# Performance work log

Measured on AMD Instinct MI355X. Metric: run time of the kernel, lower is better.

## Reference

```python
import jax, jax.numpy as jnp
import numpy as np

B, S, DA, DV, DU, L, M = 16, 256, 1, 32, 1, 4, 12


def conv1x1(x, w, b):
    # x: [B,C,H,W], w: [O,C], b: [O]
    return jnp.einsum('bchw,oc->bohw', x, w) + b[None, :, None, None]


def setup_inputs() -> dict:
    key = jax.random.key(0)
    ks = jax.random.split(key, 12)
    sc = 0.02
    return {
        'x':    jax.random.normal(ks[0], (B, S, S, DA), dtype=jnp.float32),
        'p_w':  sc * jax.random.normal(ks[1], (DV, DA + 2), dtype=jnp.float32),
        'p_b':  sc * jax.random.normal(ks[2], (DV,), dtype=jnp.float32),
        'ws_w': sc * jax.random.normal(ks[3], (L, DV, DV), dtype=jnp.float32),
        'ws_b': sc * jax.random.normal(ks[4], (L, DV), dtype=jnp.float32),
        'w1r':  sc * jax.random.normal(ks[5], (L, DV, DV, M, M), dtype=jnp.float32),
        'w1i':  sc * jax.random.normal(ks[6], (L, DV, DV, M, M), dtype=jnp.float32),
        'w2r':  sc * jax.random.normal(ks[7], (L, DV, DV, M, M), dtype=jnp.float32),
        'w2i':  sc * jax.random.normal(ks[8], (L, DV, DV, M, M), dtype=jnp.float32),
        'q_w':  sc * jax.random.normal(ks[9], (DU, DV), dtype=jnp.float32),
        'q_b':  sc * jax.random.normal(ks[10], (DU,), dtype=jnp.float32),
    }


def fourier_layer(x, w1r, w1i, w2r, w2i):
    # x: [B,C,H,W]; FFT norm None == 'backward' (numpy/jax default)
    b, c, h, w = x.shape
    x_ft = jnp.fft.rfft2(x)                       # [B,C,H,W//2+1] complex
    W1 = w1r + 1j * w1i                           # [C,C,M,M]
    W2 = w2r + 1j * w2i
    top = jnp.einsum('bixy,ioxy->boxy', x_ft[:, :, :M, :M], W1)
    bot = jnp.einsum('bixy,ioxy->boxy', x_ft[:, :, -M:, :M], W2)
    out_ft = jnp.zeros((b, c, h, w // 2 + 1), dtype=x_ft.dtype)
    out_ft = out_ft.at[:, :, :M, :M].set(top)
    out_ft = out_ft.at[:, :, h - M:, :M].set(bot)
    return jnp.fft.irfft2(out_ft, s=(h, w))


def reference(x, p_w, p_b, ws_w, ws_b, w1r, w1i, w2r, w2i, q_w, q_b):
    b, sx, sy, _ = x.shape
    # grid as in get_grid (requires sx == sy, as the original implicitly does)
    gx = jnp.linspace(-1.0, 1.0, sx, dtype=jnp.float32)
    gy = jnp.linspace(-1.0, 1.0, sy, dtype=jnp.float32)
    gridx = jnp.broadcast_to(gx.reshape(1, 1, sx, 1), (b, sy, sx, 1))
    gridy = jnp.broadcast_to(gy.reshape(1, sy, 1, 1), (b, sy, sx, 1))
    grid = jnp.concatenate([gridy, gridx], axis=-1)     # [B,Sy,Sx,2]
    h = jnp.concatenate([x, grid], axis=-1)             # [B,S,S,DA+2]
    h = jnp.transpose(h, (0, 3, 1, 2))                  # NCHW
    h = conv1x1(h, p_w, p_b)                            # lifting
    for i in range(L):
        x1 = fourier_layer(h, w1r[i], w1i[i], w2r[i], w2i[i])
        x2 = conv1x1(h, ws_w[i], ws_b[i])
        h = x1 + x2
        if i < L - 1:
            h = jax.nn.relu(h)
    h = conv1x1(h, q_w, q_b)                            # projection -> [B,1,S,S]
    return jnp.transpose(h, (0, 2, 3, 1)).squeeze(-1)   # [B,S,S]
```

## Files before the change

### kernel.cpp

```cpp
#include <hip/hip_runtime.h>
#include <math.h>

#define NB 16
#define SS 256
#define DV 32
#define MM 12
#define MK 24
#define LL 4
#define TWO_PI_N 0.024543692606170259679f


__global__ __launch_bounds__(256) void k_prep(const float* __restrict__ ws_w,
        float* __restrict__ twT, float* __restrict__ wT, float* __restrict__ tw2)
{
    int j = threadIdx.x;
    #pragma unroll
    for (int k = 0; k < MM; ++k) {
        float ang = TWO_PI_N * (float)((k * j) & 255);
        float s, c; sincosf(ang, &s, &c);
        twT[j * (MM * 2) + 2 * k]     = c;
        twT[j * (MM * 2) + 2 * k + 1] = -s;
        tw2[(k * SS + j) * 2]     = c;
        tw2[(k * SS + j) * 2 + 1] = s;
    }
    for (int idx = threadIdx.x; idx < LL * DV * DV; idx += 256) {
        int l = idx >> 10, rem = idx & 1023, co = rem >> 5, ci = rem & 31;
        wT[(l * DV + ci) * DV + co] = ws_w[(l * DV + co) * DV + ci];
    }
}

__global__ __launch_bounds__(256) void k_lift(const float* __restrict__ x,
        const float* __restrict__ p_w, const float* __restrict__ p_b,
        float* __restrict__ h)
{
    int tid = threadIdx.x;
    int lane = tid & 63;
    int w = __builtin_amdgcn_readfirstlane(tid >> 6);
    int b  = blockIdx.x >> 6;
    int iy = ((blockIdx.x & 63) << 2) + w;
    int j0 = lane << 2;

    float4 xv = *(const float4*)(x + ((size_t)(b * SS + iy)) * SS + j0);
    float gy = -1.f + 2.f * (float)iy * (1.f / 255.f);
    float4 gx;
    gx.x = -1.f + 2.f * (float)j0 * (1.f / 255.f);
    gx.y = gx.x + 2.f / 255.f; gx.z = gx.y + 2.f / 255.f; gx.w = gx.z + 2.f / 255.f;

    float* hb = h + ((size_t)b * DV * SS + iy) * SS + j0;
    #pragma unroll
    for (int c = 0; c < DV; ++c) {
        float w0 = p_w[3*c], w1 = p_w[3*c+1], w2 = p_w[3*c+2], bb = p_b[c];
        float4 v;
        v.x = w0 * xv.x + w1 * gy + w2 * gx.x + bb;
        v.y = w0 * xv.y + w1 * gy + w2 * gx.y + bb;
        v.z = w0 * xv.z + w1 * gy + w2 * gx.z + bb;
        v.w = w0 * xv.w + w1 * gy + w2 * gx.w + bb;
        *(float4*)(hb + (size_t)c * SS * SS) = v;
    }
}

__global__ __launch_bounds__(512, 4) void k_rowdft(const float* __restrict__ h,
        const float* __restrict__ twT, float* __restrict__ A)
{
    __shared__ float red[MM * 2][SS];
    int tid = threadIdx.x;
    int iy = tid & 255;
    int half = __builtin_amdgcn_readfirstlane(tid >> 8);
    int b = blockIdx.x >> 5, c = blockIdx.x & 31;

    const float4* hr = (const float4*)(h + ((size_t)blockIdx.x * SS + iy) * SS
                                         + half * 128);
    float ar[MM], ai[MM];
    #pragma unroll
    for (int k = 0; k < MM; ++k) { ar[k] = 0.f; ai[k] = 0.f; }

    #pragma unroll 4
    for (int j4 = 0; j4 < 32; ++j4) {
        float4 v = hr[j4];
        float vv[4] = {v.x, v.y, v.z, v.w};
        #pragma unroll
        for (int u = 0; u < 4; ++u) {
            const float* twj = twT + (size_t)(half * 128 + 4 * j4 + u) * (MM * 2);
            float vu = vv[u];
            #pragma unroll
            for (int k = 0; k < 6; ++k) {
                ar[2*k]   += vu * twj[4*k];
                ai[2*k]   += vu * twj[4*k + 1];
                ar[2*k+1] += vu * twj[4*k + 2];
                ai[2*k+1] += vu * twj[4*k + 3];
            }
        }
    }

    if (half == 0) {
        #pragma unroll
        for (int k = 0; k < MM; ++k) {
            red[2*k][iy]     = ar[k];
            red[2*k + 1][iy] = ai[k];
        }
    }
    __syncthreads();
    if (half == 1) {
        #pragma unroll
        for (int ky = 0; ky < MM; ++ky) {
            float2 val;
            val.x = ar[ky] + red[2*ky][iy];
            val.y = ai[ky] + red[2*ky + 1][iy];
            size_t o = ((((size_t)b * MM + ky) * DV + c) * SS + iy) * 2;
            *(float2*)&A[o] = val;
        }
    }
}

__global__ __launch_bounds__(256, 4) void k_cm(const float* __restrict__ A,
        const float* __restrict__ w1r, const float* __restrict__ w1i,
        const float* __restrict__ w2r, const float* __restrict__ w2i,
        float* __restrict__ F, int l)
{
    __shared__ float FinS[DV][6][2];
    int blk = blockIdx.x;
    int mg = blk & 3;
    int bk = blk >> 2;
    int ky = bk % MM;
    int tid = threadIdx.x;
    int c = tid >> 3, ch = tid & 7;
    int iy0 = ch * 32;

    const float2* Ap = (const float2*)(A + ((size_t)bk * DV + c) * SS * 2);

    float fr[6], fi[6], pc[6], ps[6], sc[6], ssn[6];
    #pragma unroll
    for (int k = 0; k < 6; ++k) {
        int m = mg * 6 + k;
        int f = (m < MM) ? m : (232 + m);
        float s, cc;
        sincosf(TWO_PI_N * (float)f, &s, &cc);
        sc[k] = cc; ssn[k] = s;
        sincosf(TWO_PI_N * (float)((f * iy0) & 255), &s, &cc);
        pc[k] = cc; ps[k] = s;
        fr[k] = fi[k] = 0.f;
    }
    #pragma unroll 4
    for (int i = 0; i < 32; ++i) {
        float2 a = Ap[iy0 + i];
        #pragma unroll
        for (int k = 0; k < 6; ++k) {
            fr[k] += a.x * pc[k] + a.y * ps[k];
            fi[k] += a.y * pc[k] - a.x * ps[k];
            float np = pc[k] * sc[k] - ps[k] * ssn[k];
            float nq = pc[k] * ssn[k] + ps[k] * sc[k];
            pc[k] = np; ps[k] = nq;
        }
    }
    #pragma unroll
    for (int m = 1; m < 8; m <<= 1) {
        #pragma unroll
        for (int k = 0; k < 6; ++k) {
            fr[k] += __shfl_xor(fr[k], m, 64);
            fi[k] += __shfl_xor(fi[k], m, 64);
        }
    }
    #pragma unroll
    for (int k = 0; k < 6; ++k) {
        if (ch == k) { FinS[c][k][0] = fr[k]; FinS[c][k][1] = fi[k]; }
    }
    __syncthreads();

    if (ch < 6) {
        int o = c;
        int m = mg * 6 + ch;
        const float* Wr; const float* Wi; int xm;
        if (m < MM) { Wr = w1r; Wi = w1i; xm = m; }
        else        { Wr = w2r; Wi = w2i; xm = m - MM; }
        float scale = ((ky == 0) ? 1.0f : 2.0f) * (1.0f / 65536.0f);
        float orr = 0.f, oii = 0.f;
        #pragma unroll 4
        for (int i = 0; i < DV; ++i) {
            float gr = FinS[i][ch][0], gi = FinS[i][ch][1];
            size_t wi = ((size_t)(l * DV + i) * DV + o) * (MM * MM) + xm * MM + ky;
            float wr = Wr[wi], wim = Wi[wi];
            orr += gr * wr - gi * wim;
            oii += gr * wim + gi * wr;
        }
        size_t off = (((size_t)bk * DV + o) * MK + m) * 2;
        F[off] = orr * scale; F[off + 1] = oii * scale;
    }
}

__global__ __launch_bounds__(384) void k_inv1(const float* __restrict__ F,
        float* __restrict__ g)
{
    __shared__ float itw[MK * 2];
    int tid = threadIdx.x;
    int b = blockIdx.x >> 8, iy = blockIdx.x & 255;
    if (tid < MK) {
        int f = (tid < MM) ? tid : (232 + tid);
        float ang = TWO_PI_N * (float)((f * iy) & 255);
        float s, c; sincosf(ang, &s, &c);
        itw[2 * tid] = c; itw[2 * tid + 1] = s;
    }
    __syncthreads();

    int ky = tid >> 5, co = tid & 31;
    const float2* Fp = (const float2*)(F + ((((size_t)b * MM + ky) * DV + co) * MK) * 2);
    float gr = 0.f, gi = 0.f;
    #pragma unroll
    for (int m = 0; m < MK; ++m) {
        float2 fv = Fp[m];
        float ic = itw[2 * m], is = itw[2 * m + 1];
        gr += fv.x * ic - fv.y * is;
        gi += fv.x * is + fv.y * ic;
    }
    size_t o = (((size_t)(b * SS + iy)) * MM + ky) * (DV * 2) + 2 * co;
    g[o] = gr; g[o + 1] = gi;
}

template<int FINAL>
__global__ __launch_bounds__(256, 4) void k_pt(float* __restrict__ h,
        const float* __restrict__ g, const float* __restrict__ wT,
        const float* __restrict__ ws_b, const float* __restrict__ tw2,
        const float* __restrict__ q_w, const float* __restrict__ q_b,
        float* __restrict__ out, int l)
{
    int tid = threadIdx.x;
    int lane = tid & 63;
    int w = __builtin_amdgcn_readfirstlane(tid >> 6);
    int b  = blockIdx.x >> 7;
    int iy = ((blockIdx.x & 127) << 1) + (w >> 1);
    int j0 = ((w & 1) << 7) + (lane << 1);

    float* hb = h + ((size_t)b * DV * SS + iy) * SS + j0;
    const float* wt  = wT + (size_t)l * DV * DV;
    const float* wsb = ws_b + (size_t)l * DV;

    float2 acc[DV];
    #pragma unroll
    for (int co = 0; co < DV; ++co) {
        float bv = wsb[co];
        acc[co].x = bv; acc[co].y = bv;
    }

    #pragma unroll 4
    for (int ci = 0; ci < DV; ++ci) {
        float2 hv = *(const float2*)(hb + (size_t)ci * SS * SS);
        const float* wc = wt + ci * DV;
        #pragma unroll
        for (int co = 0; co < DV; ++co) {
            float wv = wc[co];
            acc[co].x += wv * hv.x; acc[co].y += wv * hv.y;
        }
    }

    const float* gp = g + ((size_t)(b * SS + iy)) * (MM * DV * 2);
    #pragma unroll 2
    for (int ky = 0; ky < MM; ++ky) {
        float4 t4 = *(const float4*)(tw2 + ((size_t)ky * SS + j0) * 2);
        const float* Gk = gp + ky * (DV * 2);
        #pragma unroll
        for (int co = 0; co < DV; ++co) {
            float gr = Gk[2 * co], gi = Gk[2 * co + 1];
            acc[co].x += gr * t4.x - gi * t4.y;
            acc[co].y += gr * t4.z - gi * t4.w;
        }
    }

    if (FINAL) {
        float qb = q_b[0];
        float2 o2; o2.x = qb; o2.y = qb;
        #pragma unroll
        for (int co = 0; co < DV; ++co) {
            float qv = q_w[co];
            o2.x += qv * acc[co].x; o2.y += qv * acc[co].y;
        }
        *(float2*)(out + ((size_t)(b * SS + iy)) * SS + j0) = o2;
    } else {
        #pragma unroll
        for (int co = 0; co < DV; ++co) {
            float2 v;
            v.x = fmaxf(acc[co].x, 0.f); v.y = fmaxf(acc[co].y, 0.f);
            *(float2*)(hb + (size_t)co * SS * SS) = v;
        }
    }
}

extern "C" void kernel_launch(void* const* d_in, const int* in_sizes, int n_in,
                              void* d_out, int out_size, void* d_ws, size_t ws_size,
                              hipStream_t stream)
{
    const float* x    = (const float*)d_in[0];
    const float* p_w  = (const float*)d_in[1];
    const float* p_b  = (const float*)d_in[2];
    const float* ws_w = (const float*)d_in[3];
    const float* ws_b = (const float*)d_in[4];
    const float* w1r  = (const float*)d_in[5];
    const float* w1i  = (const float*)d_in[6];
    const float* w2r  = (const float*)d_in[7];
    const float* w2i  = (const float*)d_in[8];
    const float* q_w  = (const float*)d_in[9];
    const float* q_b  = (const float*)d_in[10];
    float* out = (float*)d_out;

    float* h   = (float*)d_ws;
    float* A   = h   + (size_t)NB * DV * SS * SS;
    float* F   = A   + (size_t)NB * MM * DV * SS * 2;
    float* g   = F   + (size_t)NB * MM * DV * MK * 2;
    float* twT = g   + (size_t)NB * SS * MM * DV * 2;
    float* wT  = twT + (size_t)SS * MM * 2;
    float* tw2 = wT  + (size_t)LL * DV * DV;

    dim3 blk(256);
    k_prep<<<1, blk, 0, stream>>>(ws_w, twT, wT, tw2);
    k_lift<<<NB * 64, blk, 0, stream>>>(x, p_w, p_b, h);
    for (int l = 0; l < LL; ++l) {
        k_rowdft<<<NB * DV, dim3(512), 0, stream>>>(h, twT, A);
        k_cm<<<NB * MM * 4, blk, 0, stream>>>(A, w1r, w1i, w2r, w2i, F, l);
        k_inv1<<<NB * SS, dim3(384), 0, stream>>>(F, g);
        if (l < LL - 1)
            k_pt<0><<<NB * 128, blk, 0, stream>>>(h, g, wT, ws_b, tw2,
                                                  nullptr, nullptr, nullptr, l);
        else
            k_pt<1><<<NB * 128, blk, 0, stream>>>(h, g, wT, ws_b, tw2,
                                                  q_w, q_b, out, l);
    }
}
```

Measured before the change: 737.5 us.

## Stage row-DFT input through padded LDS tiles and transpose F layout

The row DFT kernel now loads 64-column tiles of each channel plane with coalesced float4 reads into padded shared memory (stride 65), and each thread then reads its own row from LDS. Before, each thread streamed its own row directly from global memory, giving strided, uncoalesced access. The F buffer layout is also changed to [b,ky,m,co] so that k_inv1's per-m reads across co are contiguous. In exchange the kernel uses about 66KB of LDS and adds extra barriers, which may lower occupancy.

New measurement: 708.3 us. 4.0% less time.

```diff
diff --git a/kernel.cpp b/kernel.cpp
--- a/kernel.cpp
+++ b/kernel.cpp
@@ -8,6 +8,7 @@
 #define MK 24
 #define LL 4
 #define TWO_PI_N 0.024543692606170259679f
+#define TSTR 65
 
 
 __global__ __launch_bounds__(256) void k_prep(const float* __restrict__ ws_w,
@@ -62,41 +63,54 @@
 __global__ __launch_bounds__(512, 4) void k_rowdft(const float* __restrict__ h,
         const float* __restrict__ twT, float* __restrict__ A)
 {
-    __shared__ float red[MM * 2][SS];
+    __shared__ float smem[SS * TSTR];
     int tid = threadIdx.x;
     int iy = tid & 255;
     int half = __builtin_amdgcn_readfirstlane(tid >> 8);
     int b = blockIdx.x >> 5, c = blockIdx.x & 31;
-
-    const float4* hr = (const float4*)(h + ((size_t)blockIdx.x * SS + iy) * SS
-                                         + half * 128);
+    const float* hrow = h + (size_t)blockIdx.x * SS * SS;
+
     float ar[MM], ai[MM];
     #pragma unroll
     for (int k = 0; k < MM; ++k) { ar[k] = 0.f; ai[k] = 0.f; }
 
-    #pragma unroll 4
-    for (int j4 = 0; j4 < 32; ++j4) {
-        float4 v = hr[j4];
-        float vv[4] = {v.x, v.y, v.z, v.w};
-        #pragma unroll
-        for (int u = 0; u < 4; ++u) {
-            const float* twj = twT + (size_t)(half * 128 + 4 * j4 + u) * (MM * 2);
-            float vu = vv[u];
+    for (int t = 0; t < 4; ++t) {
+        int jb = t * 64;
+        __syncthreads();
+        #pragma unroll
+        for (int k = 0; k < 8; ++k) {
+            int idx = tid + k * 512;
+            int row = idx >> 4, col4 = idx & 15;
+            float4 v = *(const float4*)(hrow + (size_t)row * SS + jb + col4 * 4);
+            float* d = &smem[row * TSTR + col4 * 4];
+            d[0] = v.x; d[1] = v.y; d[2] = v.z; d[3] = v.w;
+        }
+        __syncthreads();
+        const float* rp = &smem[iy * TSTR + half * 32];
+        #pragma unroll
+        for (int jq = 0; jq < 8; ++jq) {
             #pragma unroll
-            for (int k = 0; k < 6; ++k) {
-                ar[2*k]   += vu * twj[4*k];
-                ai[2*k]   += vu * twj[4*k + 1];
-                ar[2*k+1] += vu * twj[4*k + 2];
-                ai[2*k+1] += vu * twj[4*k + 3];
+            for (int u = 0; u < 4; ++u) {
+                float v = rp[jq * 4 + u];
+                const float* twj = twT + (size_t)(jb + half * 32 + jq * 4 + u)
+                                         * (MM * 2);
+                #pragma unroll
+                for (int k = 0; k < 6; ++k) {
+                    ar[2*k]   += v * twj[4*k];
+                    ai[2*k]   += v * twj[4*k + 1];
+                    ar[2*k+1] += v * twj[4*k + 2];
+                    ai[2*k+1] += v * twj[4*k + 3];
+                }
             }
         }
     }
 
+    __syncthreads();
     if (half == 0) {
         #pragma unroll
         for (int k = 0; k < MM; ++k) {
-            red[2*k][iy]     = ar[k];
-            red[2*k + 1][iy] = ai[k];
+            smem[(2*k) * SS + iy]     = ar[k];
+            smem[(2*k + 1) * SS + iy] = ai[k];
         }
     }
     __syncthreads();
@@ -104,8 +118,8 @@
         #pragma unroll
         for (int ky = 0; ky < MM; ++ky) {
             float2 val;
-            val.x = ar[ky] + red[2*ky][iy];
-            val.y = ai[ky] + red[2*ky + 1][iy];
+            val.x = ar[ky] + smem[(2*ky) * SS + iy];
+            val.y = ai[ky] + smem[(2*ky + 1) * SS + iy];
             size_t o = ((((size_t)b * MM + ky) * DV + c) * SS + iy) * 2;
             *(float2*)&A[o] = val;
         }
@@ -182,7 +196,7 @@
             orr += gr * wr - gi * wim;
             oii += gr * wim + gi * wr;
         }
-        size_t off = (((size_t)bk * DV + o) * MK + m) * 2;
+        size_t off = (((size_t)bk * MK + m) * DV + o) * 2;
         F[off] = orr * scale; F[off + 1] = oii * scale;
     }
 }
@@ -202,11 +216,11 @@
     __syncthreads();
 
     int ky = tid >> 5, co = tid & 31;
-    const float2* Fp = (const float2*)(F + ((((size_t)b * MM + ky) * DV + co) * MK) * 2);
+    const float* Fp = F + ((size_t)(b * MM + ky) * MK) * (DV * 2) + 2 * co;
     float gr = 0.f, gi = 0.f;
     #pragma unroll
     for (int m = 0; m < MK; ++m) {
-        float2 fv = Fp[m];
+        float2 fv = *(const float2*)(Fp + (size_t)m * (DV * 2));
         float ic = itw[2 * m], is = itw[2 * m + 1];
         gr += fv.x * ic - fv.y * is;
         gi += fv.x * is + fv.y * ic;
@@ -303,7 +317,7 @@
     float* h   = (float*)d_ws;
     float* A   = h   + (size_t)NB * DV * SS * SS;
     float* F   = A   + (size_t)NB * MM * DV * SS * 2;
-    float* g   = F   + (size_t)NB * MM * DV * MK * 2;
+    float* g   = F   + (size_t)NB * MM * MK * DV * 2;
     float* twT = g   + (size_t)NB * SS * MM * DV * 2;
     float* wT  = twT + (size_t)SS * MM * 2;
     float* tw2 = wT  + (size_t)LL * DV * DV;
```
